# Performance work log

Measured on AMD Instinct MI355X. Metric: run time of the kernel, lower is better.

## Reference

```python
import jax, jax.numpy as jnp
import numpy as np


def make_dct_kernel():
    # K[u*8+v, i*8+j] = c(u)*c(v)*cos((2i+1)u*pi/16)*cos((2j+1)v*pi/16)
    # matches the torch initialize_kernel loop (kernel[index2, index]).
    r1 = np.sqrt(1.0 / 8)
    r2 = np.sqrt(2.0 / 8)
    idx = np.arange(8)
    A = np.cos(np.outer(2 * idx + 1, idx) * np.pi / 16)  # A[i, u]
    r = np.where(idx == 0, r1, r2)  # c(u)
    K4 = (r[:, None, None, None] * r[None, :, None, None]
          * A.T[:, None, :, None] * A.T[None, :, None, :])  # [u, v, i, j]
    return jnp.asarray(K4.reshape(64, 64), dtype=jnp.float32)


def setup_inputs() -> dict:
    key = jax.random.key(0)
    k1, k2 = jax.random.split(key)
    N, C, H, W = 16, 64, 256, 256
    x = jax.random.normal(k1, (N, C, H, W), dtype=jnp.float32)
    backbone = jax.random.uniform(k2, (N, 64), dtype=jnp.float32)
    it_weights = jnp.ones((64,), dtype=jnp.float32)
    return {"x": x, "backbone": backbone, "it_weights": it_weights}


def reference(x, backbone, it_weights):
    # concat_mode=0, category_num=1.
    # torch builds kernel[n*64+o, c] = K[o, c] * (backbone[n, o] * it_weights[o])
    # then applies a groups=N 1x1 conv; equivalent to a per-sample scaled
    # 64x64 channel transform per pixel:
    K = make_dct_kernel()  # [64, 64] constant buffer
    scale = backbone * it_weights[None, :]        # [N, 64]
    y = jnp.einsum('oc,nchw->nohw', K, x)         # per-pixel 64x64 matmul
    return scale[:, :, None, None] * y            # [N, 64, H, W]
```

## Files before the change

kernel.cpp:

```cpp
#include <hip/hip_runtime.h>

#define E8 0.35355339059327373f
#define C1 0.49039264020161522f
#define C3 0.41573480615127262f
#define C5 0.27778511650980114f
#define C7 0.09754516100806412f
#define D1 0.46193976625564337f
#define D3 0.19134171618254492f

static __device__ const float MK[8][8] = {
    { E8,  E8,  E8,  E8,  E8,  E8,  E8,  E8},
    { C1,  C3,  C5,  C7, -C7, -C5, -C3, -C1},
    { D1,  D3, -D3, -D1, -D1, -D3,  D3,  D1},
    { C3, -C7, -C1, -C5,  C5,  C1,  C7, -C3},
    { E8, -E8, -E8,  E8,  E8, -E8, -E8,  E8},
    { C5, -C1,  C7,  C3, -C3, -C7,  C1, -C5},
    { D3, -D1,  D1, -D3, -D3,  D1, -D1,  D3},
    { C7, -C5,  C3, -C1,  C1, -C3,  C5, -C7},
};

__global__ __launch_bounds__(256) void dct_sep_kernel(
    const float* __restrict__ x,
    const float* __restrict__ backbone,
    const float* __restrict__ itw,
    float* __restrict__ out)
{
    const int HW = 256 * 256;
    const int b = blockIdx.x;
    const int n = b >> 8;
    const int pix = ((b & 255) << 8) | threadIdx.x;

    __shared__ float s_sc[64];
    if (threadIdx.x < 64) {
        s_sc[threadIdx.x] = backbone[(n << 6) + threadIdx.x] * itw[threadIdx.x];
    }
    __syncthreads();

    const float* xp = x + (size_t)n * 64 * HW + pix;

    float xr[8][8];
#pragma unroll
    for (int i = 0; i < 8; ++i) {
#pragma unroll
        for (int j = 0; j < 8; ++j) {
            xr[i][j] = xp[(size_t)(i * 8 + j) * HW];
        }
    }

    float t[8][8];
#pragma unroll
    for (int i = 0; i < 8; ++i) {
#pragma unroll
        for (int v = 0; v < 8; ++v) {
            float a = MK[v][0] * xr[i][0];
#pragma unroll
            for (int j = 1; j < 8; ++j) {
                a = fmaf(MK[v][j], xr[i][j], a);
            }
            t[i][v] = a;
        }
    }

    float* op = out + (size_t)n * 64 * HW + pix;
#pragma unroll
    for (int u = 0; u < 8; ++u) {
#pragma unroll
        for (int v = 0; v < 8; ++v) {
            float a = MK[u][0] * t[0][v];
#pragma unroll
            for (int i = 1; i < 8; ++i) {
                a = fmaf(MK[u][i], t[i][v], a);
            }
            op[(size_t)(u * 8 + v) * HW] = a * s_sc[u * 8 + v];
        }
    }
}

extern "C" void kernel_launch(void* const* d_in, const int* in_sizes, int n_in,
                              void* d_out, int out_size, void* d_ws, size_t ws_size,
                              hipStream_t stream) {
    const float* x        = (const float*)d_in[0];
    const float* backbone = (const float*)d_in[1];
    const float* itw      = (const float*)d_in[2];
    float* out = (float*)d_out;

    dct_sep_kernel<<<4096, 256, 0, stream>>>(x, backbone, itw, out);
}
```

Baseline: 432.3 us.

## Stage input and output tiles through LDS with direct global-to-LDS 16-byte loads

```diff
diff --git a/kernel.cpp b/kernel.cpp
--- a/kernel.cpp
+++ b/kernel.cpp
@@ -19,60 +19,75 @@
     { C7, -C5,  C3, -C1,  C1, -C3,  C5, -C7},
 };
 
-__global__ __launch_bounds__(256) void dct_sep_kernel(
+typedef float f4 __attribute__((ext_vector_type(4)));
+
+__global__ __launch_bounds__(256) void dct_lds_kernel(
     const float* __restrict__ x,
     const float* __restrict__ backbone,
     const float* __restrict__ itw,
     float* __restrict__ out)
 {
-    const int HW = 256 * 256;
-    const int b = blockIdx.x;
-    const int n = b >> 8;
-    const int pix = ((b & 255) << 8) | threadIdx.x;
+    const int HW = 65536;
+    const size_t CHW = (size_t)64 * HW;
 
+    __shared__ float tile[64 * 256];
     __shared__ float s_sc[64];
-    if (threadIdx.x < 64) {
-        s_sc[threadIdx.x] = backbone[(n << 6) + threadIdx.x] * itw[threadIdx.x];
+
+    const int tid  = threadIdx.x;
+    const int n    = blockIdx.x >> 8;
+    const int px0  = (blockIdx.x & 255) << 8;
+    const int wave = tid >> 6;
+    const int lane = tid & 63;
+
+    if (tid < 64) s_sc[tid] = backbone[(n << 6) + tid] * itw[tid];
+
+    const float* gbase = x + (size_t)n * CHW + px0 + lane * 4;
+#pragma unroll
+    for (int k = 0; k < 16; ++k) {
+        const int ch = wave * 16 + k;
+        __builtin_amdgcn_global_load_lds(
+            (const __attribute__((address_space(1))) void*)(gbase + (size_t)ch * HW),
+            (__attribute__((address_space(3))) void*)(&tile[ch * 256]),
+            16, 0, 0);
     }
     __syncthreads();
 
-    const float* xp = x + (size_t)n * 64 * HW + pix;
-
-    float xr[8][8];
+    float t8[8][8];
 #pragma unroll
     for (int i = 0; i < 8; ++i) {
+        float xr[8];
 #pragma unroll
-        for (int j = 0; j < 8; ++j) {
-            xr[i][j] = xp[(size_t)(i * 8 + j) * HW];
+        for (int j = 0; j < 8; ++j) xr[j] = tile[(i * 8 + j) * 256 + tid];
+#pragma unroll
+        for (int v = 0; v < 8; ++v) {
+            float a = MK[v][0] * xr[0];
+#pragma unroll
+            for (int j = 1; j < 8; ++j) a = fmaf(MK[v][j], xr[j], a);
+            t8[i][v] = a;
         }
     }
+    __syncthreads();
 
-    float t[8][8];
-#pragma unroll
-    for (int i = 0; i < 8; ++i) {
-#pragma unroll
-        for (int v = 0; v < 8; ++v) {
-            float a = MK[v][0] * xr[i][0];
-#pragma unroll
-            for (int j = 1; j < 8; ++j) {
-                a = fmaf(MK[v][j], xr[i][j], a);
-            }
-            t[i][v] = a;
-        }
-    }
-
-    float* op = out + (size_t)n * 64 * HW + pix;
 #pragma unroll
     for (int u = 0; u < 8; ++u) {
 #pragma unroll
         for (int v = 0; v < 8; ++v) {
-            float a = MK[u][0] * t[0][v];
+            float a = MK[u][0] * t8[0][v];
 #pragma unroll
-            for (int i = 1; i < 8; ++i) {
-                a = fmaf(MK[u][i], t[i][v], a);
-            }
-            op[(size_t)(u * 8 + v) * HW] = a * s_sc[u * 8 + v];
+            for (int i = 1; i < 8; ++i) a = fmaf(MK[u][i], t8[i][v], a);
+            tile[(u * 8 + v) * 256 + tid] = a;
         }
+    }
+    __syncthreads();
+
+    float* obase = out + (size_t)n * CHW + px0 + lane * 4;
+#pragma unroll
+    for (int k = 0; k < 16; ++k) {
+        const int ch = wave * 16 + k;
+        f4 r = *(const f4*)&tile[ch * 256 + lane * 4];
+        const float s = s_sc[ch];
+        r.x *= s; r.y *= s; r.z *= s; r.w *= s;
+        *(f4*)(obase + (size_t)ch * HW) = r;
     }
 }
 
@@ -84,5 +99,5 @@
     const float* itw      = (const float*)d_in[2];
     float* out = (float*)d_out;
 
-    dct_sep_kernel<<<4096, 256, 0, stream>>>(x, backbone, itw, out);
+    dct_lds_kernel<<<4096, 256, 0, stream>>>(x, backbone, itw, out);
 }
```

New measurement: 429.8 us. No clear change (-0.6%).
